# Optimization experiments

Hardware: AMD Instinct MI355X
Metric: run time of the kernel (lower is better)

Reference implementation:

```python
import jax, jax.numpy as jnp
import numpy as np


def setup_inputs() -> dict:
    key = jax.random.key(0)
    k1, k2, k3, k4, k5 = jax.random.split(key, 5)
    B, T, C = 64, 1024, 768
    scale = 1.0 / np.sqrt(C)
    tokens = jax.random.normal(k1, (B, T, C), dtype=jnp.float32)
    mask_topk = jax.random.randint(k2, (B, T), 0, 2) > 0
    Wq = jax.random.normal(k3, (C, C), dtype=jnp.float32) * scale
    Wk = jax.random.normal(k4, (C, C), dtype=jnp.float32) * scale
    Wv = jax.random.normal(k5, (C, C), dtype=jnp.float32) * scale
    return {"tokens": tokens, "mask_topk": mask_topk, "Wq": Wq, "Wk": Wk, "Wv": Wv}


def reference(tokens, mask_topk, Wq, Wk, Wv):
    # tokens: [B, T, C]; mask_topk: [B, T] bool; W*: [C, C] (torch Linear weight, y = x @ W.T)
    C = tokens.shape[-1]
    m = mask_topk.astype(tokens.dtype)                      # [B, T]
    cnt = jnp.sum(m, axis=-1, keepdims=True)                # [B, 1]
    masked_sum = jnp.einsum('btc,bt->bc', tokens, m)        # [B, C]
    mean_all = jnp.mean(tokens, axis=1)                     # fallback when mask is empty
    q_sal = jnp.where(cnt > 0, masked_sum / jnp.maximum(cnt, 1.0), mean_all)  # [B, C]
    q_sal = q_sal[:, None, :]                               # [B, 1, C]

    Q = jnp.einsum('bqc,dc->bqd', q_sal, Wq)                # [B, 1, C]
    K = jnp.einsum('btc,dc->btd', tokens, Wk)               # [B, T, C]
    V = jnp.einsum('btc,dc->btd', tokens, Wv)               # [B, T, C]

    scores = jnp.einsum('bqd,btd->bqt', Q, K) / jnp.sqrt(jnp.asarray(C, tokens.dtype))
    attn = jax.nn.softmax(scores, axis=-1)                  # [B, 1, T]
    v_fg = jnp.einsum('bqt,btd->bqd', attn, V)[:, 0, :]     # [B, C]
    return (v_fg, attn)
```

## Files before the change

### kernel.cpp

```cpp
#include <hip/hip_runtime.h>
#include <hip/hip_bf16.h>

#define B 64
#define T 1024
#define C 768
#define TSPLIT 32
#define TCHUNK (T / TSPLIT)

#define OFF_MSUM   64
#define OFF_ASUM   (OFF_MSUM + B*TSPLIT*C)
#define OFF_CNT    (OFF_ASUM + B*TSPLIT*C)
#define OFF_Q      (OFF_CNT + B*TSPLIT)
#define OFF_QK     (OFF_Q + B*C)
#define OFF_SCORES (OFF_QK + B*C)
#define OFF_MPART  (OFF_SCORES + B*T)
#define OFF_SPART  (OFF_MPART + B*TSPLIT)
#define OFF_PPART  (OFF_SPART + B*TSPLIT)

__device__ __forceinline__ bool read_mask(const void* mask, int mode, int idx) {
    if (mode == 1) return ((const unsigned char*)mask)[idx] != 0;
    if (mode == 2) return ((const float*)mask)[idx] != 0.0f;
    return ((const int*)mask)[idx] != 0;
}

__global__ void k_detect(const void* mask, int* mode_out) {
    __shared__ int s_not01, s_isf;
    int tid = threadIdx.x;
    if (tid == 0) { s_not01 = 0; s_isf = 0; }
    __syncthreads();
    const int* mi = (const int*)mask;
    int not01 = 0, isf = 0;
    for (int k = 0; k < 64; ++k) {
        int v = mi[tid + 256 * k];
        if (v != 0 && v != 1) not01 = 1;
        if (v == 0x3F800000) isf = 1;
    }
    if (not01) atomicOr(&s_not01, 1);
    if (isf)   atomicOr(&s_isf, 1);
    __syncthreads();
    if (tid == 0) *mode_out = s_isf ? 2 : (s_not01 ? 1 : 0);
}

__global__ __launch_bounds__(192) void
k_pass1(const float* __restrict__ tokens, const void* mask, const int* modep,
        float* __restrict__ msum, float* __restrict__ asum, float* __restrict__ cntpart) {
    int ts = blockIdx.x, b = blockIdx.y, tid = threadIdx.x;
    int mode = *modep;
    __shared__ float s_m[TCHUNK];
    if (tid < TCHUNK)
        s_m[tid] = read_mask(mask, mode, b * T + ts * TCHUNK + tid) ? 1.f : 0.f;
    __syncthreads();
    int c = tid * 4;
    float4 ms = {0, 0, 0, 0}, as = {0, 0, 0, 0};
    const float* tb = tokens + (size_t)b * T * C;
#pragma unroll 4
    for (int r = 0; r < TCHUNK; ++r) {
        int t = ts * TCHUNK + r;
        float4 x = *(const float4*)(tb + (size_t)t * C + c);
        as.x += x.x; as.y += x.y; as.z += x.z; as.w += x.w;
        float wm = s_m[r];
        ms.x += wm * x.x; ms.y += wm * x.y; ms.z += wm * x.z; ms.w += wm * x.w;
    }
    size_t o = (size_t)(b * TSPLIT + ts) * C + c;
    *(float4*)(msum + o) = ms;
    *(float4*)(asum + o) = as;
    if (tid == 0) {
        float cnt = 0.f;
#pragma unroll
        for (int r = 0; r < TCHUNK; ++r) cnt += s_m[r];
        cntpart[b * TSPLIT + ts] = cnt;
    }
}

__global__ __launch_bounds__(256) void
k_qsal_rowdot(const float* __restrict__ msum, const float* __restrict__ asum,
              const float* __restrict__ cntpart, const float* __restrict__ Wq,
              float* __restrict__ Qv) {
    int b = blockIdx.y, tid = threadIdx.x;
    __shared__ float sq[C];
    float cnt = 0.f;
#pragma unroll
    for (int p = 0; p < TSPLIT; ++p) cnt += cntpart[b * TSPLIT + p];
    bool um = (cnt > 0.f);
    float scale = um ? (1.f / fmaxf(cnt, 1.f)) : (1.f / (float)T);
    const float* src = um ? msum : asum;
    for (int c = tid; c < C; c += 256) {
        float a = 0.f;
#pragma unroll 8
        for (int p = 0; p < TSPLIT; ++p) a += src[(size_t)(b * TSPLIT + p) * C + c];
        sq[c] = a * scale;
    }
    __syncthreads();
    int d = blockIdx.x * 64 + (tid >> 2), sub = tid & 3;
    const float4* w = (const float4*)(Wq + (size_t)d * C);
    const float4* v4 = (const float4*)sq;
    float acc = 0.f;
#pragma unroll 8
    for (int j = sub * 48; j < sub * 48 + 48; ++j) {
        float4 a = v4[j], x = w[j];
        acc += a.x * x.x + a.y * x.y + a.z * x.z + a.w * x.w;
    }
    acc += __shfl_xor(acc, 1);
    acc += __shfl_xor(acc, 2);
    if (sub == 0) Qv[b * C + d] = acc;
}

__global__ __launch_bounds__(256) void
k_coldot(const float* __restrict__ Qv, const float* __restrict__ Wk,
         float* __restrict__ qk) {
    int b = blockIdx.y, tid = threadIdx.x;
    __shared__ float sQ[C];
    for (int c = tid; c < C; c += 256) sQ[c] = Qv[b * C + c];
    __syncthreads();
    int c = blockIdx.x * 64 + (tid >> 2), sub = tid & 3;
    float acc = 0.f;
#pragma unroll 8
    for (int i = 0; i < 192; ++i) {
        int d = sub * 192 + i;
        acc += sQ[d] * Wk[(size_t)d * C + c];
    }
    acc += __shfl_xor(acc, 1);
    acc += __shfl_xor(acc, 2);
    if (sub == 0) qk[b * C + c] = acc * 0.03608439182435161f;
}

__global__ __launch_bounds__(192) void
k_fused(const float* __restrict__ tokens, const float* __restrict__ qk,
        float* __restrict__ scores, float* __restrict__ mpart,
        float* __restrict__ spart, float* __restrict__ ppart) {
    __shared__ float sq[C];
    __shared__ float ssc[TCHUNK];
    __shared__ float sw[TCHUNK];
    int ts = blockIdx.x, b = blockIdx.y, tid = threadIdx.x;
    ((float4*)sq)[tid] = ((const float4*)(qk + (size_t)b * C))[tid];
    __syncthreads();
    int wave = tid >> 6, lane = tid & 63;
    const float* tb = tokens + (size_t)b * T * C;
    const float4* q4 = (const float4*)sq;
    for (int r = wave; r < TCHUNK; r += 3) {
        int t = ts * TCHUNK + r;
        const float4* row = (const float4*)(tb + (size_t)t * C);
        float acc = 0.f;
#pragma unroll
        for (int j = 0; j < 3; ++j) {
            int idx = lane + 64 * j;
            float4 x = row[idx], q = q4[idx];
            acc += x.x * q.x + x.y * q.y + x.z * q.z + x.w * q.w;
        }
        for (int s = 32; s > 0; s >>= 1) acc += __shfl_xor(acc, s);
        if (lane == 0) { ssc[r] = acc; scores[(size_t)b * T + t] = acc; }
    }
    __syncthreads();
    float m = -3.4e38f;
#pragma unroll
    for (int r = 0; r < TCHUNK; ++r) m = fmaxf(m, ssc[r]);
    if (tid < TCHUNK) sw[tid] = expf(ssc[tid] - m);
    __syncthreads();
    float s = 0.f;
#pragma unroll
    for (int r = 0; r < TCHUNK; ++r) s += sw[r];
    int c = tid * 4;
    float4 acc = {0, 0, 0, 0};
#pragma unroll 4
    for (int r = 0; r < TCHUNK; ++r) {
        int t = ts * TCHUNK + r;
        float wv = sw[r];
        float4 x = *(const float4*)(tb + (size_t)t * C + c);
        acc.x += wv * x.x; acc.y += wv * x.y; acc.z += wv * x.z; acc.w += wv * x.w;
    }
    *(float4*)(ppart + (size_t)(b * TSPLIT + ts) * C + c) = acc;
    if (tid == 0) { mpart[b * TSPLIT + ts] = m; spart[b * TSPLIT + ts] = s; }
}

__global__ __launch_bounds__(256) void
k_vfg_attn(const float* __restrict__ ppart, const float* __restrict__ scores,
           const float* __restrict__ mpart, const float* __restrict__ spart,
           const float* __restrict__ Wv, float* __restrict__ vfg,
           float* __restrict__ attn) {
    int bx = blockIdx.x, b = blockIdx.y, tid = threadIdx.x;
    float M = -3.4e38f;
#pragma unroll
    for (int p = 0; p < TSPLIT; ++p) M = fmaxf(M, mpart[b * TSPLIT + p]);
    float Z = 0.f;
#pragma unroll
    for (int p = 0; p < TSPLIT; ++p) Z += spart[b * TSPLIT + p] * expf(mpart[b * TSPLIT + p] - M);
    float invZ = 1.f / Z;
    if (bx == 12) {
        float4 sc = ((const float4*)(scores + (size_t)b * T))[tid];
        float4 o;
        o.x = expf(sc.x - M) * invZ; o.y = expf(sc.y - M) * invZ;
        o.z = expf(sc.z - M) * invZ; o.w = expf(sc.w - M) * invZ;
        ((float4*)(attn + (size_t)b * T))[tid] = o;
        return;
    }
    __shared__ float sp[C];
    float coef[TSPLIT];
#pragma unroll
    for (int p = 0; p < TSPLIT; ++p) coef[p] = expf(mpart[b * TSPLIT + p] - M) * invZ;
    for (int c = tid; c < C; c += 256) {
        float a = 0.f;
#pragma unroll 8
        for (int p = 0; p < TSPLIT; ++p)
            a += coef[p] * ppart[(size_t)(b * TSPLIT + p) * C + c];
        sp[c] = a;
    }
    __syncthreads();
    int d = bx * 64 + (tid >> 2), sub = tid & 3;
    const float4* w = (const float4*)(Wv + (size_t)d * C);
    const float4* v4 = (const float4*)sp;
    float acc = 0.f;
#pragma unroll 8
    for (int j = sub * 48; j < sub * 48 + 48; ++j) {
        float4 a = v4[j], x = w[j];
        acc += a.x * x.x + a.y * x.y + a.z * x.z + a.w * x.w;
    }
    acc += __shfl_xor(acc, 1);
    acc += __shfl_xor(acc, 2);
    if (sub == 0) vfg[b * C + d] = acc;
}

extern "C" void kernel_launch(void* const* d_in, const int* in_sizes, int n_in,
                              void* d_out, int out_size, void* d_ws, size_t ws_size,
                              hipStream_t stream) {
    const float* tokens = (const float*)d_in[0];
    const void*  mask   = d_in[1];
    const float* Wq     = (const float*)d_in[2];
    const float* Wk     = (const float*)d_in[3];
    const float* Wv     = (const float*)d_in[4];

    float* ws      = (float*)d_ws;
    int*   mode    = (int*)d_ws;
    float* msum    = ws + OFF_MSUM;
    float* asum    = ws + OFF_ASUM;
    float* cntpart = ws + OFF_CNT;
    float* Qv      = ws + OFF_Q;
    float* qk      = ws + OFF_QK;
    float* scores  = ws + OFF_SCORES;
    float* mpart   = ws + OFF_MPART;
    float* spart   = ws + OFF_SPART;
    float* ppart   = ws + OFF_PPART;

    float* v_fg = (float*)d_out;
    float* attn = (float*)d_out + B * C;

    k_detect<<<1, 256, 0, stream>>>(mask, mode);
    k_pass1<<<dim3(TSPLIT, B), 192, 0, stream>>>(tokens, mask, mode, msum, asum, cntpart);
    k_qsal_rowdot<<<dim3(12, B), 256, 0, stream>>>(msum, asum, cntpart, Wq, Qv);
    k_coldot<<<dim3(12, B), 256, 0, stream>>>(Qv, Wk, qk);
    k_fused<<<dim3(TSPLIT, B), 192, 0, stream>>>(tokens, qk, scores, mpart, spart, ppart);
    k_vfg_attn<<<dim3(13, B), 256, 0, stream>>>(ppart, scores, mpart, spart, Wv, v_fg, attn);
}
```

Baseline: 174.1 us.

## Drop unmasked-sum partials, compute fallback mean lazily, widen fused kernel to four waves

Pass 1 no longer accumulates and writes the all-token partial sums. The empty-mask fallback now recomputes the mean directly from tokens inside the Q kernel, and only when that fallback is needed. This removes a large partial-sum write and read from the common path, at the cost of a slow serial path when a batch's mask is empty. The fused score kernel moves to 256 threads so four waves compute row dots, with only 192 threads doing the weighted sum. The mask-format detection also reads fewer words.

```diff
diff --git a/kernel.cpp b/kernel.cpp
--- a/kernel.cpp
+++ b/kernel.cpp
@@ -8,8 +8,7 @@
 #define TCHUNK (T / TSPLIT)
 
 #define OFF_MSUM   64
-#define OFF_ASUM   (OFF_MSUM + B*TSPLIT*C)
-#define OFF_CNT    (OFF_ASUM + B*TSPLIT*C)
+#define OFF_CNT    (OFF_MSUM + B*TSPLIT*C)
 #define OFF_Q      (OFF_CNT + B*TSPLIT)
 #define OFF_QK     (OFF_Q + B*C)
 #define OFF_SCORES (OFF_QK + B*C)
@@ -30,7 +29,8 @@
     __syncthreads();
     const int* mi = (const int*)mask;
     int not01 = 0, isf = 0;
-    for (int k = 0; k < 64; ++k) {
+#pragma unroll
+    for (int k = 0; k < 16; ++k) {
         int v = mi[tid + 256 * k];
         if (v != 0 && v != 1) not01 = 1;
         if (v == 0x3F800000) isf = 1;
@@ -43,7 +43,7 @@
 
 __global__ __launch_bounds__(192) void
 k_pass1(const float* __restrict__ tokens, const void* mask, const int* modep,
-        float* __restrict__ msum, float* __restrict__ asum, float* __restrict__ cntpart) {
+        float* __restrict__ msum, float* __restrict__ cntpart) {
     int ts = blockIdx.x, b = blockIdx.y, tid = threadIdx.x;
     int mode = *modep;
     __shared__ float s_m[TCHUNK];
@@ -51,19 +51,16 @@
         s_m[tid] = read_mask(mask, mode, b * T + ts * TCHUNK + tid) ? 1.f : 0.f;
     __syncthreads();
     int c = tid * 4;
-    float4 ms = {0, 0, 0, 0}, as = {0, 0, 0, 0};
+    float4 ms = {0, 0, 0, 0};
     const float* tb = tokens + (size_t)b * T * C;
 #pragma unroll 4
     for (int r = 0; r < TCHUNK; ++r) {
         int t = ts * TCHUNK + r;
         float4 x = *(const float4*)(tb + (size_t)t * C + c);
-        as.x += x.x; as.y += x.y; as.z += x.z; as.w += x.w;
         float wm = s_m[r];
         ms.x += wm * x.x; ms.y += wm * x.y; ms.z += wm * x.z; ms.w += wm * x.w;
     }
-    size_t o = (size_t)(b * TSPLIT + ts) * C + c;
-    *(float4*)(msum + o) = ms;
-    *(float4*)(asum + o) = as;
+    *(float4*)(msum + (size_t)(b * TSPLIT + ts) * C + c) = ms;
     if (tid == 0) {
         float cnt = 0.f;
 #pragma unroll
@@ -73,22 +70,29 @@
 }
 
 __global__ __launch_bounds__(256) void
-k_qsal_rowdot(const float* __restrict__ msum, const float* __restrict__ asum,
-              const float* __restrict__ cntpart, const float* __restrict__ Wq,
+k_qsal_rowdot(const float* __restrict__ msum, const float* __restrict__ cntpart,
+              const float* __restrict__ tokens, const float* __restrict__ Wq,
               float* __restrict__ Qv) {
     int b = blockIdx.y, tid = threadIdx.x;
     __shared__ float sq[C];
     float cnt = 0.f;
 #pragma unroll
     for (int p = 0; p < TSPLIT; ++p) cnt += cntpart[b * TSPLIT + p];
-    bool um = (cnt > 0.f);
-    float scale = um ? (1.f / fmaxf(cnt, 1.f)) : (1.f / (float)T);
-    const float* src = um ? msum : asum;
-    for (int c = tid; c < C; c += 256) {
-        float a = 0.f;
-#pragma unroll 8
-        for (int p = 0; p < TSPLIT; ++p) a += src[(size_t)(b * TSPLIT + p) * C + c];
-        sq[c] = a * scale;
+    if (cnt > 0.f) {
+        float scale = 1.f / cnt;
+        for (int c = tid; c < C; c += 256) {
+            float a = 0.f;
+#pragma unroll 8
+            for (int p = 0; p < TSPLIT; ++p) a += msum[(size_t)(b * TSPLIT + p) * C + c];
+            sq[c] = a * scale;
+        }
+    } else {
+        const float* tb = tokens + (size_t)b * T * C;
+        for (int c = tid; c < C; c += 256) {
+            float a = 0.f;
+            for (int t = 0; t < T; ++t) a += tb[(size_t)t * C + c];
+            sq[c] = a * (1.f / (float)T);
+        }
     }
     __syncthreads();
     int d = blockIdx.x * 64 + (tid >> 2), sub = tid & 3;
@@ -124,7 +128,7 @@
     if (sub == 0) qk[b * C + c] = acc * 0.03608439182435161f;
 }
 
-__global__ __launch_bounds__(192) void
+__global__ __launch_bounds__(256) void
 k_fused(const float* __restrict__ tokens, const float* __restrict__ qk,
         float* __restrict__ scores, float* __restrict__ mpart,
         float* __restrict__ spart, float* __restrict__ ppart) {
@@ -132,12 +136,14 @@
     __shared__ float ssc[TCHUNK];
     __shared__ float sw[TCHUNK];
     int ts = blockIdx.x, b = blockIdx.y, tid = threadIdx.x;
-    ((float4*)sq)[tid] = ((const float4*)(qk + (size_t)b * C))[tid];
+    if (tid < 192) ((float4*)sq)[tid] = ((const float4*)(qk + (size_t)b * C))[tid];
     __syncthreads();
     int wave = tid >> 6, lane = tid & 63;
     const float* tb = tokens + (size_t)b * T * C;
     const float4* q4 = (const float4*)sq;
-    for (int r = wave; r < TCHUNK; r += 3) {
+#pragma unroll
+    for (int rr = 0; rr < TCHUNK / 4; ++rr) {
+        int r = rr * 4 + wave;
         int t = ts * TCHUNK + r;
         const float4* row = (const float4*)(tb + (size_t)t * C);
         float acc = 0.f;
@@ -156,20 +162,25 @@
     for (int r = 0; r < TCHUNK; ++r) m = fmaxf(m, ssc[r]);
     if (tid < TCHUNK) sw[tid] = expf(ssc[tid] - m);
     __syncthreads();
-    float s = 0.f;
-#pragma unroll
-    for (int r = 0; r < TCHUNK; ++r) s += sw[r];
-    int c = tid * 4;
-    float4 acc = {0, 0, 0, 0};
+    if (tid < 192) {
+        int c = tid * 4;
+        float4 acc = {0, 0, 0, 0};
 #pragma unroll 4
-    for (int r = 0; r < TCHUNK; ++r) {
-        int t = ts * TCHUNK + r;
-        float wv = sw[r];
-        float4 x = *(const float4*)(tb + (size_t)t * C + c);
-        acc.x += wv * x.x; acc.y += wv * x.y; acc.z += wv * x.z; acc.w += wv * x.w;
-    }
-    *(float4*)(ppart + (size_t)(b * TSPLIT + ts) * C + c) = acc;
-    if (tid == 0) { mpart[b * TSPLIT + ts] = m; spart[b * TSPLIT + ts] = s; }
+        for (int r = 0; r < TCHUNK; ++r) {
+            int t = ts * TCHUNK + r;
+            float wv = sw[r];
+            float4 x = *(const float4*)(tb + (size_t)t * C + c);
+            acc.x += wv * x.x; acc.y += wv * x.y; acc.z += wv * x.z; acc.w += wv * x.w;
+        }
+        *(float4*)(ppart + (size_t)(b * TSPLIT + ts) * C + c) = acc;
+    }
+    if (tid == 0) {
+        float s = 0.f;
+#pragma unroll
+        for (int r = 0; r < TCHUNK; ++r) s += sw[r];
+        mpart[b * TSPLIT + ts] = m;
+        spart[b * TSPLIT + ts] = s;
+    }
 }
 
 __global__ __launch_bounds__(256) void
@@ -231,7 +242,6 @@
     float* ws      = (float*)d_ws;
     int*   mode    = (int*)d_ws;
     float* msum    = ws + OFF_MSUM;
-    float* asum    = ws + OFF_ASUM;
     float* cntpart = ws + OFF_CNT;
     float* Qv      = ws + OFF_Q;
     float* qk      = ws + OFF_QK;
@@ -244,9 +254,9 @@
     float* attn = (float*)d_out + B * C;
 
     k_detect<<<1, 256, 0, stream>>>(mask, mode);
-    k_pass1<<<dim3(TSPLIT, B), 192, 0, stream>>>(tokens, mask, mode, msum, asum, cntpart);
-    k_qsal_rowdot<<<dim3(12, B), 256, 0, stream>>>(msum, asum, cntpart, Wq, Qv);
+    k_pass1<<<dim3(TSPLIT, B), 192, 0, stream>>>(tokens, mask, mode, msum, cntpart);
+    k_qsal_rowdot<<<dim3(12, B), 256, 0, stream>>>(msum, cntpart, tokens, Wq, Qv);
     k_coldot<<<dim3(12, B), 256, 0, stream>>>(Qv, Wk, qk);
-    k_fused<<<dim3(TSPLIT, B), 192, 0, stream>>>(tokens, qk, scores, mpart, spart, ppart);
+    k_fused<<<dim3(TSPLIT, B), 256, 0, stream>>>(tokens, qk, scores, mpart, spart, ppart);
     k_vfg_attn<<<dim3(13, B), 256, 0, stream>>>(ppart, scores, mpart, spart, Wv, v_fg, attn);
 }
```

Result: no change. 172.5 us (-0.9%).
